# Optimization experiments

Hardware: AMD Instinct MI355X
Metric: run time of the kernel (lower is better)

## Reference

```python
import jax, jax.numpy as jnp
import numpy as np

N = 25000        # nodes
E = 400000       # edges
MUL = 64         # multiplicity per irrep
NB = 8           # number_of_basis
RN = 64          # radial_neurons
NUM_NEIGH = 16.0
INV_SQRT3 = 1.0 / np.sqrt(3.0)


def setup_inputs() -> dict:
    key = jax.random.key(0)
    ks = jax.random.split(key, 14)
    f32 = jnp.float32
    return {
        "node_input": jax.random.normal(ks[0], (N, 4 * MUL), f32),          # 64x0e + 64x1o
        "node_attr": jnp.ones((N, 1), f32),                                  # 1x0e
        "edge_src": jax.random.randint(ks[1], (E,), 0, N, dtype=jnp.int32),
        "edge_dst": jax.random.randint(ks[2], (E,), 0, N, dtype=jnp.int32),
        "edge_attr": jax.random.normal(ks[3], (E, 4), f32),                  # SH: 1x0e + 1x1o
        "edge_length_embedded": jax.random.uniform(ks[4], (E, NB), f32),
        # FullyConnectedTensorProduct weights (scalar node attr -> per-irrep channel mixing)
        "W_sc0": jax.random.normal(ks[5], (MUL, MUL), f32),
        "W_sc1": jax.random.normal(ks[6], (MUL, MUL), f32),
        "W_lin1_0": jax.random.normal(ks[7], (MUL, MUL), f32),
        "W_lin1_1": jax.random.normal(ks[8], (MUL, MUL), f32),
        # radial MLP: [NB] -> [RN] -> [tp.weight_numel = 4*MUL]
        "fc_w0": jax.random.normal(ks[9], (NB, RN), f32),
        "fc_w1": jax.random.normal(ks[10], (RN, 4 * MUL), f32),
        "W_lin2_0": jax.random.normal(ks[11], (2 * MUL, MUL), f32),
        "W_lin2_1": jax.random.normal(ks[12], (2 * MUL, MUL), f32),
    }


def _forward(node_input, node_attr, edge_attr, edge_length_embedded,
             W_sc0, W_sc1, W_lin1_0, W_lin1_1, fc_w0, fc_w1, W_lin2_0, W_lin2_1,
             edge_src, edge_dst):
    Nn = node_input.shape[0]
    z = node_attr                                   # [N,1] scalar attr
    x0 = node_input[:, :MUL]                        # [N,64]   0e
    x1 = node_input[:, MUL:].reshape(Nn, MUL, 3)    # [N,64,3] 1o
    inv_m = 1.0 / np.sqrt(MUL)
    # self-connection sc = FCTP(in, attr, out); scalar attr -> per-irrep linear * z / sqrt(fan)
    s0 = (x0 @ W_sc0) * z * inv_m
    s1 = jnp.einsum('nuc,uv->nvc', x1, W_sc1) * z[:, :, None] * inv_m
    # lin1
    h0 = (x0 @ W_lin1_0) * z * inv_m
    h1 = jnp.einsum('nuc,uv->nvc', x1, W_lin1_1) * z[:, :, None] * inv_m
    # radial network: silu hidden, linear out, 1/sqrt(fan_in) weight norm
    hid = jax.nn.silu((edge_length_embedded @ fc_w0) / np.sqrt(NB))
    w = (hid @ fc_w1) / np.sqrt(RN)                 # [E, 4*MUL] per-edge TP weights
    wA, wB, wC, wD = w[:, :MUL], w[:, MUL:2 * MUL], w[:, 2 * MUL:3 * MUL], w[:, 3 * MUL:]
    # gather source node features per edge
    xs0 = h0[edge_src]                              # [E,64]
    xs1 = h1[edge_src]                              # [E,64,3]
    sh0 = edge_attr[:, :1]                          # [E,1]
    sh1 = edge_attr[:, 1:4]                         # [E,3]
    # CG tensor product paths ('uvu', edge mult = 1)
    midA = wA * xs0 * sh0                                           # 0e x 0e -> 0e
    midD = wD * jnp.einsum('euc,ec->eu', xs1, sh1) * INV_SQRT3       # 1o x 1o -> 0e
    midB = (wB * xs0)[:, :, None] * sh1[:, None, :]                  # 0e x 1o -> 1o
    midC = wC[:, :, None] * xs1 * sh0[:, None, :]                    # 1o x 0e -> 1o
    mid0 = jnp.concatenate([midA, midD], axis=1)                     # [E,128]
    mid1 = jnp.concatenate([midB, midC], axis=1)                     # [E,128,3]
    # scatter-add to destination nodes, / sqrt(num_neighbors)
    inv_nb = 1.0 / np.sqrt(NUM_NEIGH)
    y0 = jax.ops.segment_sum(mid0, edge_dst, num_segments=Nn) * inv_nb
    y1 = jax.ops.segment_sum(mid1.reshape(mid1.shape[0], -1), edge_dst,
                             num_segments=Nn).reshape(Nn, 2 * MUL, 3) * inv_nb
    # lin2: mix the two 0e blocks -> 64x0e, two 1o blocks -> 64x1o
    inv_2m = 1.0 / np.sqrt(2 * MUL)
    o0 = (y0 @ W_lin2_0) * z * inv_2m
    o1 = jnp.einsum('nuc,uv->nvc', y1, W_lin2_1) * z[:, :, None] * inv_2m
    # sc output_mask is all ones here (every output irrep has an sc path)
    c_s = np.float32(np.sin(np.pi / 8.0))
    c_x = np.float32(np.cos(np.pi / 8.0))
    out0 = c_s * s0 + c_x * o0
    out1 = c_s * s1 + c_x * o1
    return jnp.concatenate([out0, out1.reshape(Nn, 3 * MUL)], axis=1)


def reference(node_input, node_attr, edge_src, edge_dst, edge_attr, edge_length_embedded,
              W_sc0, W_sc1, W_lin1_0, W_lin1_1, fc_w0, fc_w1, W_lin2_0, W_lin2_1):
    return _forward(node_input, node_attr, edge_attr, edge_length_embedded,
                    W_sc0, W_sc1, W_lin1_0, W_lin1_1, fc_w0, fc_w1, W_lin2_0, W_lin2_1,
                    edge_src, edge_dst)
```

## Files before the change

kernel.cpp:

```cpp
#include <hip/hip_runtime.h>
#include <math.h>

#define NN 25000
#define NE 400000

#define C_S 0.3826834323650898f
#define C_X 0.9238795325112867f
#define INV_SQRT3 0.5773502691896258f
#define INV_M 0.125f
#define INV_2M 0.08838834764831845f
#define INV_NB 0.25f
#define INV_SQRT_NB 0.3535533905932738f

__global__ __launch_bounds__(512) void node_linear1(
    const float* __restrict__ node_input, const float* __restrict__ node_attr,
    const float* __restrict__ W_sc0, const float* __restrict__ W_sc1,
    const float* __restrict__ W_l10, const float* __restrict__ W_l11,
    float* __restrict__ out, float* __restrict__ hbuf)
{
    __shared__ float xrow[64];
    __shared__ float xT[192];
    __shared__ float orow[256];
    __shared__ float hrow[256];
    const int tid = threadIdx.x;
    const int wave = tid >> 6;
    const int lane = tid & 63;
    const float* Wm;
    int chan = 0;
    if (wave == 0)      Wm = W_sc0;
    else if (wave == 1) Wm = W_l10;
    else if (wave <= 4) { Wm = W_sc1; chan = wave - 2; }
    else                { Wm = W_l11; chan = wave - 5; }
    float wcol[64];
#pragma unroll
    for (int u = 0; u < 64; ++u) wcol[u] = Wm[u * 64 + lane];

    for (int n = blockIdx.x; n < NN; n += gridDim.x) {
        if (tid < 64) xrow[tid] = node_input[n * 256 + tid];
        else if (tid < 256) {
            float v = node_input[n * 256 + tid];
            int j = tid - 64;
            xT[(j % 3) * 64 + (j / 3)] = v;
        }
        __syncthreads();
        float z = node_attr[n];
        const float* xv = (wave < 2) ? xrow : (xT + chan * 64);
        float acc = 0.f;
#pragma unroll
        for (int u = 0; u < 64; u += 4) {
            float4 x4 = *reinterpret_cast<const float4*>(xv + u);
            acc = fmaf(x4.x, wcol[u + 0], acc);
            acc = fmaf(x4.y, wcol[u + 1], acc);
            acc = fmaf(x4.z, wcol[u + 2], acc);
            acc = fmaf(x4.w, wcol[u + 3], acc);
        }
        acc *= INV_M * z;
        if (wave == 0)      orow[lane] = C_S * acc;
        else if (wave == 1) hrow[lane * 4 + 0] = acc;
        else if (wave <= 4) orow[64 + lane * 3 + chan] = C_S * acc;
        else                hrow[lane * 4 + 1 + chan] = acc;
        __syncthreads();
        if (tid < 256) out[n * 256 + tid] = orow[tid];
        else           hbuf[n * 256 + (tid - 256)] = hrow[tid - 256];
        __syncthreads();
    }
}

__global__ void zero_counts(int* counts) {
    int i = blockIdx.x * blockDim.x + threadIdx.x;
    if (i < NN) counts[i] = 0;
}
__global__ void hist_kernel(const int* __restrict__ edge_dst, int* __restrict__ counts) {
    for (int i = blockIdx.x * blockDim.x + threadIdx.x; i < NE; i += gridDim.x * blockDim.x)
        atomicAdd(&counts[edge_dst[i]], 1);
}
__global__ __launch_bounds__(1024) void scan_kernel(const int* __restrict__ counts,
                                                    int* __restrict__ row_start,
                                                    int* __restrict__ cursor)
{
    __shared__ int partial[1024];
    const int tid = threadIdx.x;
    const int CH = 25;
    int begin = tid * CH;
    int end = begin + CH; if (end > NN) end = NN;
    if (begin > NN) begin = NN;
    int s = 0;
    for (int i = begin; i < end; ++i) s += counts[i];
    partial[tid] = s;
    __syncthreads();
    for (int off = 1; off < 1024; off <<= 1) {
        int v = partial[tid];
        int a = (tid >= off) ? partial[tid - off] : 0;
        __syncthreads();
        partial[tid] = v + a;
        __syncthreads();
    }
    int run = (tid > 0) ? partial[tid - 1] : 0;
    for (int i = begin; i < end; ++i) {
        row_start[i] = run;
        cursor[i] = run;
        run += counts[i];
    }
    if (tid == 1023) row_start[NN] = partial[1023];
}
__global__ void scatter_kernel(const int* __restrict__ edge_dst, int* __restrict__ cursor,
                               int* __restrict__ csr) {
    for (int i = blockIdx.x * blockDim.x + threadIdx.x; i < NE; i += gridDim.x * blockDim.x) {
        int p = atomicAdd(&cursor[edge_dst[i]], 1);
        csr[p] = i;
    }
}

__global__ __launch_bounds__(512) void edge_reduce(
    const float* __restrict__ elemb, const float* __restrict__ edge_attr,
    const float* __restrict__ fc_w0, const float* __restrict__ fc_w1,
    const int* __restrict__ edge_src,
    const int* __restrict__ csr, const int* __restrict__ row_start,
    const float* __restrict__ hbuf, float* __restrict__ ybuf)
{
    __shared__ float fcw1p[16384];
    __shared__ float hidb[8][512];
    const int tid = threadIdx.x, wave = tid >> 6, lane = tid & 63;
    for (int i = tid; i < 16384; i += 512) {
        int v = i >> 8, j = i & 255, k = j >> 6, u = j & 63;
        fcw1p[v * 256 + u * 4 + k] = fc_w1[i] * 0.125f;
    }
    float fw0[8];
#pragma unroll
    for (int b = 0; b < 8; ++b) fw0[b] = fc_w0[b * 64 + lane];
    __syncthreads();

    for (int n = blockIdx.x * 8 + wave; n < NN; n += gridDim.x * 8) {
        int row = __builtin_amdgcn_readfirstlane(row_start[n]);
        int cnt = __builtin_amdgcn_readfirstlane(row_start[n + 1]) - row;
        float accA = 0.f, accD = 0.f;
        float accB0 = 0.f, accB1 = 0.f, accB2 = 0.f;
        float accC0 = 0.f, accC1 = 0.f, accC2 = 0.f;
        for (int base = 0; base < cnt; base += 8) {
            int e[8];
            float hid[8];
#pragma unroll
            for (int ee = 0; ee < 8; ++ee) {
                if (base + ee < cnt) {
                    int ev = __builtin_amdgcn_readfirstlane(csr[row + base + ee]);
                    e[ee] = ev;
                    float4 b0 = *reinterpret_cast<const float4*>(elemb + (long)ev * 8);
                    float4 b1 = *reinterpret_cast<const float4*>(elemb + (long)ev * 8 + 4);
                    float d = b0.x * fw0[0] + b0.y * fw0[1] + b0.z * fw0[2] + b0.w * fw0[3]
                            + b1.x * fw0[4] + b1.y * fw0[5] + b1.z * fw0[6] + b1.w * fw0[7];
                    d *= INV_SQRT_NB;
                    hid[ee] = d / (1.f + __expf(-d));
                } else {
                    e[ee] = 0;
                    hid[ee] = 0.f;
                }
            }
            *reinterpret_cast<float4*>(&hidb[wave][lane * 8]) =
                make_float4(hid[0], hid[1], hid[2], hid[3]);
            *reinterpret_cast<float4*>(&hidb[wave][lane * 8 + 4]) =
                make_float4(hid[4], hid[5], hid[6], hid[7]);
            float4 xs[4], sh[4];
#pragma unroll
            for (int ee = 0; ee < 4; ++ee) {
                int src = __builtin_amdgcn_readfirstlane(edge_src[e[ee]]);
                xs[ee] = *reinterpret_cast<const float4*>(hbuf + (long)src * 256 + lane * 4);
                sh[ee] = *reinterpret_cast<const float4*>(edge_attr + (long)e[ee] * 4);
            }
            float wAc[8] = {0,0,0,0,0,0,0,0}, wBc[8] = {0,0,0,0,0,0,0,0};
            float wCc[8] = {0,0,0,0,0,0,0,0}, wDc[8] = {0,0,0,0,0,0,0,0};
#pragma unroll 8
            for (int v = 0; v < 64; ++v) {
                float4 wv = *reinterpret_cast<const float4*>(&fcw1p[v * 256 + lane * 4]);
                float4 h0 = *reinterpret_cast<const float4*>(&hidb[wave][v * 8]);
                float4 h1 = *reinterpret_cast<const float4*>(&hidb[wave][v * 8 + 4]);
                float ha[8] = {h0.x, h0.y, h0.z, h0.w, h1.x, h1.y, h1.z, h1.w};
#pragma unroll
                for (int ee = 0; ee < 8; ++ee) {
                    wAc[ee] = fmaf(wv.x, ha[ee], wAc[ee]);
                    wBc[ee] = fmaf(wv.y, ha[ee], wBc[ee]);
                    wCc[ee] = fmaf(wv.z, ha[ee], wCc[ee]);
                    wDc[ee] = fmaf(wv.w, ha[ee], wDc[ee]);
                }
            }
            float4 xs2[4], sh2[4];
#pragma unroll
            for (int ee = 0; ee < 4; ++ee) {
                int src = __builtin_amdgcn_readfirstlane(edge_src[e[ee + 4]]);
                xs2[ee] = *reinterpret_cast<const float4*>(hbuf + (long)src * 256 + lane * 4);
                sh2[ee] = *reinterpret_cast<const float4*>(edge_attr + (long)e[ee + 4] * 4);
            }
#pragma unroll
            for (int ee = 0; ee < 4; ++ee) {
                float x0 = xs[ee].x, x1a = xs[ee].y, x1b = xs[ee].z, x1c = xs[ee].w;
                float s0 = sh[ee].x, s1x = sh[ee].y, s1y = sh[ee].z, s1z = sh[ee].w;
                accA = fmaf(wAc[ee] * x0, s0, accA);
                float dot3 = x1a * s1x + x1b * s1y + x1c * s1z;
                accD = fmaf(wDc[ee], dot3, accD);
                float wbx = wBc[ee] * x0;
                accB0 = fmaf(wbx, s1x, accB0);
                accB1 = fmaf(wbx, s1y, accB1);
                accB2 = fmaf(wbx, s1z, accB2);
                float wcs = wCc[ee] * s0;
                accC0 = fmaf(wcs, x1a, accC0);
                accC1 = fmaf(wcs, x1b, accC1);
                accC2 = fmaf(wcs, x1c, accC2);
            }
#pragma unroll
            for (int ee = 0; ee < 4; ++ee) {
                float x0 = xs2[ee].x, x1a = xs2[ee].y, x1b = xs2[ee].z, x1c = xs2[ee].w;
                float s0 = sh2[ee].x, s1x = sh2[ee].y, s1y = sh2[ee].z, s1z = sh2[ee].w;
                accA = fmaf(wAc[ee + 4] * x0, s0, accA);
                float dot3 = x1a * s1x + x1b * s1y + x1c * s1z;
                accD = fmaf(wDc[ee + 4], dot3, accD);
                float wbx = wBc[ee + 4] * x0;
                accB0 = fmaf(wbx, s1x, accB0);
                accB1 = fmaf(wbx, s1y, accB1);
                accB2 = fmaf(wbx, s1z, accB2);
                float wcs = wCc[ee + 4] * s0;
                accC0 = fmaf(wcs, x1a, accC0);
                accC1 = fmaf(wcs, x1b, accC1);
                accC2 = fmaf(wcs, x1c, accC2);
            }
        }
        float* yr = ybuf + (long)n * 512;
        yr[lane]       = accA * INV_NB;
        yr[64 + lane]  = accD * (INV_NB * INV_SQRT3);
        yr[128 + lane] = accB0 * INV_NB;
        yr[192 + lane] = accC0 * INV_NB;
        yr[256 + lane] = accB1 * INV_NB;
        yr[320 + lane] = accC1 * INV_NB;
        yr[384 + lane] = accB2 * INV_NB;
        yr[448 + lane] = accC2 * INV_NB;
    }
}

__global__ __launch_bounds__(256) void node_linear2(
    const float* __restrict__ ybuf, const float* __restrict__ node_attr,
    const float* __restrict__ W20, const float* __restrict__ W21,
    float* __restrict__ out)
{
    __shared__ float yrow[512];
    const int tid = threadIdx.x, wave = tid >> 6, lane = tid & 63;
    const float* Wm = (wave == 0) ? W20 : W21;
    float wc[128];
#pragma unroll
    for (int j = 0; j < 128; ++j) wc[j] = Wm[j * 64 + lane];
    for (int n = blockIdx.x; n < NN; n += gridDim.x) {
        yrow[tid]       = ybuf[(long)n * 512 + tid];
        yrow[256 + tid] = ybuf[(long)n * 512 + 256 + tid];
        __syncthreads();
        float z = node_attr[n];
        const float* yv = (wave == 0) ? yrow : (yrow + 128 + (wave - 1) * 128);
        float acc = 0.f;
#pragma unroll
        for (int j = 0; j < 128; j += 4) {
            float4 y4 = *reinterpret_cast<const float4*>(yv + j);
            acc = fmaf(y4.x, wc[j + 0], acc);
            acc = fmaf(y4.y, wc[j + 1], acc);
            acc = fmaf(y4.z, wc[j + 2], acc);
            acc = fmaf(y4.w, wc[j + 3], acc);
        }
        acc *= C_X * INV_2M * z;
        int oidx = (wave == 0) ? (n * 256 + lane) : (n * 256 + 64 + lane * 3 + (wave - 1));
        out[oidx] += acc;
        __syncthreads();
    }
}

extern "C" void kernel_launch(void* const* d_in, const int* in_sizes, int n_in,
                              void* d_out, int out_size, void* d_ws, size_t ws_size,
                              hipStream_t stream)
{
    (void)in_sizes; (void)n_in; (void)out_size; (void)ws_size;
    const float* node_input = (const float*)d_in[0];
    const float* node_attr  = (const float*)d_in[1];
    const int*   edge_src   = (const int*)d_in[2];
    const int*   edge_dst   = (const int*)d_in[3];
    const float* edge_attr  = (const float*)d_in[4];
    const float* elemb      = (const float*)d_in[5];
    const float* W_sc0      = (const float*)d_in[6];
    const float* W_sc1      = (const float*)d_in[7];
    const float* W_l10      = (const float*)d_in[8];
    const float* W_l11      = (const float*)d_in[9];
    const float* fc_w0      = (const float*)d_in[10];
    const float* fc_w1      = (const float*)d_in[11];
    const float* W20        = (const float*)d_in[12];
    const float* W21        = (const float*)d_in[13];
    float* out = (float*)d_out;

    float* hbuf = (float*)d_ws;
    float* ybuf = hbuf + (size_t)NN * 256;
    int* counts    = (int*)(ybuf + (size_t)NN * 512);
    int* row_start = counts + NN;
    int* cursor    = row_start + NN + 8;
    int* csr       = cursor + NN;

    node_linear1<<<1024, 512, 0, stream>>>(node_input, node_attr, W_sc0, W_sc1,
                                           W_l10, W_l11, out, hbuf);
    zero_counts<<<(NN + 255) / 256, 256, 0, stream>>>(counts);
    hist_kernel<<<1024, 256, 0, stream>>>(edge_dst, counts);
    scan_kernel<<<1, 1024, 0, stream>>>(counts, row_start, cursor);
    scatter_kernel<<<1024, 256, 0, stream>>>(edge_dst, cursor, csr);
    edge_reduce<<<512, 512, 0, stream>>>(elemb, edge_attr, fc_w0, fc_w1, edge_src,
                                         csr, row_start, hbuf, ybuf);
    node_linear2<<<1024, 256, 0, stream>>>(ybuf, node_attr, W20, W21, out);
}
```

Before: 608.9 us.

## Raise occupancy: split lin2 K-dim across waves, double edge_reduce grid

Result: slower. 622.9 us (+2.3%).

```diff
diff --git a/kernel.cpp b/kernel.cpp
--- a/kernel.cpp
+++ b/kernel.cpp
@@ -111,7 +111,7 @@
     }
 }
 
-__global__ __launch_bounds__(512) void edge_reduce(
+__global__ __launch_bounds__(512, 2) void edge_reduce(
     const float* __restrict__ elemb, const float* __restrict__ edge_attr,
     const float* __restrict__ fc_w0, const float* __restrict__ fc_w1,
     const int* __restrict__ edge_src,
@@ -234,35 +234,42 @@
     }
 }
 
-__global__ __launch_bounds__(256) void node_linear2(
+__global__ __launch_bounds__(512) void node_linear2(
     const float* __restrict__ ybuf, const float* __restrict__ node_attr,
     const float* __restrict__ W20, const float* __restrict__ W21,
     float* __restrict__ out)
 {
     __shared__ float yrow[512];
+    __shared__ float ppart[8][64];
     const int tid = threadIdx.x, wave = tid >> 6, lane = tid & 63;
-    const float* Wm = (wave == 0) ? W20 : W21;
-    float wc[128];
-#pragma unroll
-    for (int j = 0; j < 128; ++j) wc[j] = Wm[j * 64 + lane];
+    const int role = wave >> 1, half = wave & 1;
+    const float* Wm = (role == 0) ? W20 : W21;
+    float wcol[64];
+#pragma unroll
+    for (int k = 0; k < 64; ++k) wcol[k] = Wm[(half * 64 + k) * 64 + lane];
+
     for (int n = blockIdx.x; n < NN; n += gridDim.x) {
-        yrow[tid]       = ybuf[(long)n * 512 + tid];
-        yrow[256 + tid] = ybuf[(long)n * 512 + 256 + tid];
-        __syncthreads();
-        float z = node_attr[n];
-        const float* yv = (wave == 0) ? yrow : (yrow + 128 + (wave - 1) * 128);
+        yrow[tid] = ybuf[(size_t)n * 512 + tid];
+        __syncthreads();
+        const float* yv = (role == 0) ? yrow : (yrow + 128 + (role - 1) * 128);
+        const float* yh = yv + half * 64;
         float acc = 0.f;
 #pragma unroll
-        for (int j = 0; j < 128; j += 4) {
-            float4 y4 = *reinterpret_cast<const float4*>(yv + j);
-            acc = fmaf(y4.x, wc[j + 0], acc);
-            acc = fmaf(y4.y, wc[j + 1], acc);
-            acc = fmaf(y4.z, wc[j + 2], acc);
-            acc = fmaf(y4.w, wc[j + 3], acc);
-        }
-        acc *= C_X * INV_2M * z;
-        int oidx = (wave == 0) ? (n * 256 + lane) : (n * 256 + 64 + lane * 3 + (wave - 1));
-        out[oidx] += acc;
+        for (int k = 0; k < 64; k += 4) {
+            float4 y4 = *(const float4*)(yh + k);
+            acc = fmaf(y4.x, wcol[k + 0], acc);
+            acc = fmaf(y4.y, wcol[k + 1], acc);
+            acc = fmaf(y4.z, wcol[k + 2], acc);
+            acc = fmaf(y4.w, wcol[k + 3], acc);
+        }
+        ppart[wave][lane] = acc;
+        __syncthreads();
+        if (half == 0) {
+            float z = node_attr[n];
+            float r = (ppart[wave][lane] + ppart[wave + 1][lane]) * (C_X * INV_2M) * z;
+            int oidx = (role == 0) ? lane : (64 + lane * 3 + (role - 1));
+            out[(size_t)n * 256 + oidx] += r;
+        }
         __syncthreads();
     }
 }
@@ -295,13 +302,13 @@
     int* cursor    = row_start + NN + 8;
     int* csr       = cursor + NN;
 
-    node_linear1<<<1024, 512, 0, stream>>>(node_input, node_attr, W_sc0, W_sc1,
+    node_linear1<<<2048, 512, 0, stream>>>(node_input, node_attr, W_sc0, W_sc1,
                                            W_l10, W_l11, out, hbuf);
     zero_counts<<<(NN + 255) / 256, 256, 0, stream>>>(counts);
     hist_kernel<<<1024, 256, 0, stream>>>(edge_dst, counts);
     scan_kernel<<<1, 1024, 0, stream>>>(counts, row_start, cursor);
     scatter_kernel<<<1024, 256, 0, stream>>>(edge_dst, cursor, csr);
-    edge_reduce<<<512, 512, 0, stream>>>(elemb, edge_attr, fc_w0, fc_w1, edge_src,
-                                         csr, row_start, hbuf, ybuf);
-    node_linear2<<<1024, 256, 0, stream>>>(ybuf, node_attr, W20, W21, out);
-}
+    edge_reduce<<<1024, 512, 0, stream>>>(elemb, edge_attr, fc_w0, fc_w1, edge_src,
+                                          csr, row_start, hbuf, ybuf);
+    node_linear2<<<1024, 512, 0, stream>>>(ybuf, node_attr, W20, W21, out);
+}
```
